# Optimization experiments

Hardware: AMD Instinct MI355X
Metric: run time of the kernel (lower is better)

The kernel has to match this reference:

```python
import jax, jax.numpy as jnp
import numpy as np

POOL = 7          # cfg.POOLING_SIZE
STRIDE = 16.0     # cfg.RPN_ANCHOR_STRIDE (y and x)


def _bilinear_sample(fm, py, px):
    """grid_sample (bilinear, zero padding, align_corners=True) for one image.
    fm: [C,H,W]; py, px: [R,Ho,Wo] pixel-space coords. Returns [C,R,Ho,Wo]."""
    C, H, W = fm.shape
    x0 = jnp.floor(px); y0 = jnp.floor(py)
    x1 = x0 + 1.0;      y1 = y0 + 1.0
    wx1 = px - x0; wx0 = 1.0 - wx1
    wy1 = py - y0; wy0 = 1.0 - wy1
    fm_flat = fm.reshape(C, H * W)

    def gather(y, x):
        valid = (x >= 0) & (x <= W - 1) & (y >= 0) & (y <= H - 1)
        xi = jnp.clip(x, 0, W - 1).astype(jnp.int32)
        yi = jnp.clip(y, 0, H - 1).astype(jnp.int32)
        v = jnp.take(fm_flat, (yi * W + xi).reshape(-1), axis=1)
        return v.reshape((C,) + y.shape) * valid.astype(fm.dtype)

    return (gather(y0, x0) * (wy0 * wx0) + gather(y0, x1) * (wy0 * wx1)
          + gather(y1, x0) * (wy1 * wx0) + gather(y1, x1) * (wy1 * wx1))


def setup_inputs() -> dict:
    key = jax.random.key(0)
    k1, k2, k3 = jax.random.split(key, 3)
    N, R, C, H, W = 4, 256, 1024, 50, 50
    # boxes (y, x, h, w) in original image coords (800x800 image, stride 16)
    yx = jax.random.uniform(k1, (N, R, 2), jnp.float32, 0.0, 600.0)
    hw = jax.random.uniform(k2, (N, R, 2), jnp.float32, 32.0, 200.0)
    rois = jnp.concatenate([yx, hw], axis=-1)
    feature_map = jax.random.normal(k3, (N, C, H, W), jnp.float32)
    return {"rois": rois, "feature_map": feature_map}


def reference(rois, feature_map):
    N, C, H, W = feature_map.shape
    R = rois.shape[1]
    y1 = rois[:, :, 0] / STRIDE
    x1 = rois[:, :, 1] / STRIDE
    y2 = (rois[:, :, 0] + rois[:, :, 2]) / STRIDE
    x2 = (rois[:, :, 1] + rois[:, :, 3]) / STRIDE
    # affine theta (align_corners=True convention, matching the (W-1) formulas)
    a  = (x2 - x1) / (W - 1)
    tx = (x1 + x2 - W + 1) / (W - 1)
    b  = (y2 - y1) / (H - 1)
    ty = (y1 + y2 - H + 1) / (H - 1)
    Ho = Wo = POOL * 2
    gx = jnp.linspace(-1.0, 1.0, Wo).astype(rois.dtype)
    gy = jnp.linspace(-1.0, 1.0, Ho).astype(rois.dtype)
    xs = a[:, :, None, None] * gx[None, None, None, :] + tx[:, :, None, None]  # [N,R,1,Wo]
    ys = b[:, :, None, None] * gy[None, None, :, None] + ty[:, :, None, None]  # [N,R,Ho,1]
    # normalized -> pixel coords (align_corners=True)
    px = jnp.broadcast_to((xs + 1.0) * (W - 1) / 2.0, (N, R, Ho, Wo))
    py = jnp.broadcast_to((ys + 1.0) * (H - 1) / 2.0, (N, R, Ho, Wo))
    sampled = jax.vmap(_bilinear_sample)(feature_map, py, px)  # [N,C,R,Ho,Wo]
    crops = jnp.transpose(sampled, (0, 2, 1, 3, 4))            # [N,R,C,Ho,Wo]
    crops = crops.reshape(N, R, C, POOL, 2, POOL, 2).max(axis=(4, 6))
    return crops  # [N,R,C,7,7]
```

## Files before the change

### kernel.cpp

```cpp
#include <hip/hip_runtime.h>
#include <math.h>

static constexpr int N_ = 4, R_ = 256, C_ = 1024, H_ = 50, W_ = 50, P_ = 7;
static constexpr int HW_ = H_ * W_;
static constexpr int PP_ = P_ * P_;
static constexpr int CHB_ = 4;
static constexpr int WVS_ = 16;
static constexpr int PLW_ = 2816;
static constexpr int NTASK = R_ * PP_;
static constexpr int NIT = NTASK / 64;
static constexpr int FM_WORDS = N_ * C_ * HW_;

typedef const __attribute__((address_space(1))) void* gaddr_t;
typedef __attribute__((address_space(3))) void* laddr_t;

__device__ __forceinline__ void ld_lds16(const float* g, float* l) {
    __builtin_amdgcn_global_load_lds((gaddr_t)g, (laddr_t)l, 16, 0, 0);
}

__device__ __forceinline__ void axis_w(float p0, float p1, int L,
                                       int& i0c, float wA[2], float wB[3]) {
    float f0 = floorf(p0); int i0 = (int)f0; float a0 = p0 - f0;
    float f1 = floorf(p1); int i1 = (int)f1; float a1 = p1 - f1;
    const bool o = (i1 > i0);
    wA[0] = 1.0f - a0; wA[1] = a0;
    wB[0] = o ? 0.0f : (1.0f - a1);
    wB[1] = o ? (1.0f - a1) : a1;
    wB[2] = o ? a1 : 0.0f;
    if (i0 > L - 1)     { wA[0] = 0.0f; wB[0] = 0.0f; }
    if (i0 + 1 > L - 1) { wA[1] = 0.0f; wB[1] = 0.0f; }
    if (i0 + 2 > L - 1) {               wB[2] = 0.0f; }
    i0c = min(max(i0, 0), L - 1);
}

__device__ __forceinline__ float gather9(const float* __restrict__ g,
                                         const float wyA[2], const float wyB[3],
                                         const float wxA[2], const float wxB[3]) {
    const float v00 = g[0],       v01 = g[1],          v02 = g[2];
    const float v10 = g[W_],      v11 = g[W_ + 1],     v12 = g[W_ + 2];
    const float v20 = g[2 * W_],  v21 = g[2 * W_ + 1], v22 = g[2 * W_ + 2];

    const float tA0 = fmaf(wyA[1], v10, wyA[0] * v00);
    const float tA1 = fmaf(wyA[1], v11, wyA[0] * v01);
    const float tA2 = fmaf(wyA[1], v12, wyA[0] * v02);
    const float tB0 = fmaf(wyB[2], v20, fmaf(wyB[1], v10, wyB[0] * v00));
    const float tB1 = fmaf(wyB[2], v21, fmaf(wyB[1], v11, wyB[0] * v01));
    const float tB2 = fmaf(wyB[2], v22, fmaf(wyB[1], v12, wyB[0] * v02));

    const float s00 = fmaf(wxA[1], tA1, wxA[0] * tA0);
    const float s01 = fmaf(wxB[2], tA2, fmaf(wxB[1], tA1, wxB[0] * tA0));
    const float s10 = fmaf(wxA[1], tB1, wxA[0] * tB0);
    const float s11 = fmaf(wxB[2], tB2, fmaf(wxB[1], tB1, wxB[0] * tB0));

    return fmaxf(fmaxf(s00, s01), fmaxf(s10, s11));
}

__global__ __launch_bounds__(1024, 8) void roipool_kernel(
    const float* __restrict__ rois,
    const float* __restrict__ fm,
    float* __restrict__ out) {

    __shared__ float planes[CHB_][PLW_];

    const int b  = blockIdx.x;
    const int n  = b >> 8;
    const int c0 = (b & 255) * CHB_;
    const int lane = threadIdx.x & 63;
    const int wv = __builtin_amdgcn_readfirstlane(threadIdx.x >> 6);

    {
        const int pl = wv >> 2;
        const int qh = wv & 3;
        const int base = (n * C_ + c0 + pl) * HW_;
        float* dst = &planes[pl][0];
        const int t0 = qh * 3, t1 = min(t0 + 3, 11);
        for (int t = t0; t < t1; ++t) {
            const int src = min(base + t * 256 + lane * 4, FM_WORDS - 4);
            ld_lds16(fm + src, dst + t * 256);
        }
    }
    asm volatile("s_waitcnt vmcnt(0)" ::: "memory");
    __syncthreads();

    const float* const p0l = &planes[0][0];
    const float* const p1l = &planes[1][0];
    const float* const p2l = &planes[2][0];
    const float* const p3l = &planes[3][0];

    const float4* __restrict__ rois4 = reinterpret_cast<const float4*>(rois) + n * R_;
    const size_t obase = ((size_t)n * R_ * C_ + c0) * PP_;

    for (int it = wv; it < NIT; it += WVS_) {
        const int t  = (it << 6) | lane;
        const int ri = (int)((unsigned)t / 49u);
        const int px = t - ri * 49;
        const int pi = (int)((unsigned)px / 7u);
        const int pj = px - pi * 7;

        const float4 roi = rois4[ri];
        const float y1 = roi.x * 0.0625f;
        const float x1 = roi.y * 0.0625f;
        const float y2 = (roi.x + roi.z) * 0.0625f;
        const float x2 = (roi.y + roi.w) * 0.0625f;
        const float sy = (y2 - y1) * (1.0f / 13.0f);
        const float sx = (x2 - x1) * (1.0f / 13.0f);

        const float py0 = y1 + sy * (float)(2 * pi);
        const float py1 = y1 + sy * (float)(2 * pi + 1);
        const float px0 = x1 + sx * (float)(2 * pj);
        const float px1 = x1 + sx * (float)(2 * pj + 1);

        int iy0; float wyA[2], wyB[3];
        axis_w(py0, py1, H_, iy0, wyA, wyB);
        int ix0; float wxA[2], wxB[3];
        axis_w(px0, px1, W_, ix0, wxA, wxB);
        const int gb = iy0 * W_ + ix0;

        const float r0 = gather9(p0l + gb, wyA, wyB, wxA, wxB);
        const float r1 = gather9(p1l + gb, wyA, wyB, wxA, wxB);
        const float r2 = gather9(p2l + gb, wyA, wyB, wxA, wxB);
        const float r3 = gather9(p3l + gb, wyA, wyB, wxA, wxB);

        float* __restrict__ po = out + obase + (size_t)ri * C_ * PP_ + px;
        po[0]       = r0;
        po[PP_]     = r1;
        po[2 * PP_] = r2;
        po[3 * PP_] = r3;
    }
}

extern "C" void kernel_launch(void* const* d_in, const int* in_sizes, int n_in,
                              void* d_out, int out_size, void* d_ws, size_t ws_size,
                              hipStream_t stream) {
    const float* rois = (const float*)d_in[0];
    const float* fm   = (const float*)d_in[1];
    float* out        = (float*)d_out;

    const int blocks = N_ * (C_ / CHB_);
    roipool_kernel<<<blocks, 1024, 0, stream>>>(rois, fm, out);
}
```

Measured before the change: 77.42 us.

## Interleave four channels as float4 in LDS and halve block size

Feature-map planes are staged in LDS interleaved by channel as float4, so each of the 9 taps is read with one 128-bit LDS load covering all four channels instead of four scalar loads. The async global_load_lds staging is replaced by ordinary strided global loads that the threads pack into float4 themselves. Block size drops from 1024 to 512 threads with 8 waves, which doubles the per-wave loop trip count. This trades a heavier, non-async staging phase for fewer LDS instructions in the gather loop.

```diff
diff --git a/kernel.cpp b/kernel.cpp
--- a/kernel.cpp
+++ b/kernel.cpp
@@ -5,18 +5,10 @@
 static constexpr int HW_ = H_ * W_;
 static constexpr int PP_ = P_ * P_;
 static constexpr int CHB_ = 4;
-static constexpr int WVS_ = 16;
-static constexpr int PLW_ = 2816;
+static constexpr int WVS_ = 8;
+static constexpr int P4_ = 2608;
 static constexpr int NTASK = R_ * PP_;
 static constexpr int NIT = NTASK / 64;
-static constexpr int FM_WORDS = N_ * C_ * HW_;
-
-typedef const __attribute__((address_space(1))) void* gaddr_t;
-typedef __attribute__((address_space(3))) void* laddr_t;
-
-__device__ __forceinline__ void ld_lds16(const float* g, float* l) {
-    __builtin_amdgcn_global_load_lds((gaddr_t)g, (laddr_t)l, 16, 0, 0);
-}
 
 __device__ __forceinline__ void axis_w(float p0, float p1, int L,
                                        int& i0c, float wA[2], float wB[3]) {
@@ -33,59 +25,33 @@
     i0c = min(max(i0, 0), L - 1);
 }
 
-__device__ __forceinline__ float gather9(const float* __restrict__ g,
-                                         const float wyA[2], const float wyB[3],
-                                         const float wxA[2], const float wxB[3]) {
-    const float v00 = g[0],       v01 = g[1],          v02 = g[2];
-    const float v10 = g[W_],      v11 = g[W_ + 1],     v12 = g[W_ + 2];
-    const float v20 = g[2 * W_],  v21 = g[2 * W_ + 1], v22 = g[2 * W_ + 2];
-
-    const float tA0 = fmaf(wyA[1], v10, wyA[0] * v00);
-    const float tA1 = fmaf(wyA[1], v11, wyA[0] * v01);
-    const float tA2 = fmaf(wyA[1], v12, wyA[0] * v02);
-    const float tB0 = fmaf(wyB[2], v20, fmaf(wyB[1], v10, wyB[0] * v00));
-    const float tB1 = fmaf(wyB[2], v21, fmaf(wyB[1], v11, wyB[0] * v01));
-    const float tB2 = fmaf(wyB[2], v22, fmaf(wyB[1], v12, wyB[0] * v02));
-
-    const float s00 = fmaf(wxA[1], tA1, wxA[0] * tA0);
-    const float s01 = fmaf(wxB[2], tA2, fmaf(wxB[1], tA1, wxB[0] * tA0));
-    const float s10 = fmaf(wxA[1], tB1, wxA[0] * tB0);
-    const float s11 = fmaf(wxB[2], tB2, fmaf(wxB[1], tB1, wxB[0] * tB0));
-
-    return fmaxf(fmaxf(s00, s01), fmaxf(s10, s11));
-}
-
-__global__ __launch_bounds__(1024, 8) void roipool_kernel(
+__global__ __launch_bounds__(512) void roipool_kernel(
     const float* __restrict__ rois,
     const float* __restrict__ fm,
     float* __restrict__ out) {
 
-    __shared__ float planes[CHB_][PLW_];
+    __shared__ float4 sh4[P4_];
 
     const int b  = blockIdx.x;
     const int n  = b >> 8;
     const int c0 = (b & 255) * CHB_;
-    const int lane = threadIdx.x & 63;
-    const int wv = __builtin_amdgcn_readfirstlane(threadIdx.x >> 6);
+    const int tid = threadIdx.x;
+    const int lane = tid & 63;
+    const int wv = __builtin_amdgcn_readfirstlane(tid >> 6);
 
     {
-        const int pl = wv >> 2;
-        const int qh = wv & 3;
-        const int base = (n * C_ + c0 + pl) * HW_;
-        float* dst = &planes[pl][0];
-        const int t0 = qh * 3, t1 = min(t0 + 3, 11);
-        for (int t = t0; t < t1; ++t) {
-            const int src = min(base + t * 256 + lane * 4, FM_WORDS - 4);
-            ld_lds16(fm + src, dst + t * 256);
+        const int gpb = (n * C_ + c0) * HW_;
+        for (int p = tid; p < P4_; p += 512) {
+            const int sp = min(p, HW_ - 1);
+            float4 v;
+            v.x = fm[gpb + sp];
+            v.y = fm[gpb + HW_ + sp];
+            v.z = fm[gpb + 2 * HW_ + sp];
+            v.w = fm[gpb + 3 * HW_ + sp];
+            sh4[p] = v;
         }
     }
-    asm volatile("s_waitcnt vmcnt(0)" ::: "memory");
     __syncthreads();
-
-    const float* const p0l = &planes[0][0];
-    const float* const p1l = &planes[1][0];
-    const float* const p2l = &planes[2][0];
-    const float* const p3l = &planes[3][0];
 
     const float4* __restrict__ rois4 = reinterpret_cast<const float4*>(rois) + n * R_;
     const size_t obase = ((size_t)n * R_ * C_ + c0) * PP_;
@@ -107,19 +73,39 @@
 
         const float py0 = y1 + sy * (float)(2 * pi);
         const float py1 = y1 + sy * (float)(2 * pi + 1);
-        const float px0 = x1 + sx * (float)(2 * pj);
-        const float px1 = x1 + sx * (float)(2 * pj + 1);
+        const float qx0 = x1 + sx * (float)(2 * pj);
+        const float qx1 = x1 + sx * (float)(2 * pj + 1);
 
         int iy0; float wyA[2], wyB[3];
         axis_w(py0, py1, H_, iy0, wyA, wyB);
         int ix0; float wxA[2], wxB[3];
-        axis_w(px0, px1, W_, ix0, wxA, wxB);
+        axis_w(qx0, qx1, W_, ix0, wxA, wxB);
         const int gb = iy0 * W_ + ix0;
 
-        const float r0 = gather9(p0l + gb, wyA, wyB, wxA, wxB);
-        const float r1 = gather9(p1l + gb, wyA, wyB, wxA, wxB);
-        const float r2 = gather9(p2l + gb, wyA, wyB, wxA, wxB);
-        const float r3 = gather9(p3l + gb, wyA, wyB, wxA, wxB);
+        const float4* __restrict__ G = sh4 + gb;
+        const float4 v00 = G[0],       v01 = G[1],          v02 = G[2];
+        const float4 v10 = G[W_],      v11 = G[W_ + 1],     v12 = G[W_ + 2];
+        const float4 v20 = G[2 * W_],  v21 = G[2 * W_ + 1], v22 = G[2 * W_ + 2];
+
+        float r0, r1, r2, r3;
+#define REDUCE_CH(CMP, RES) do {                                               \
+        const float tA0 = fmaf(wyA[1], v10.CMP, wyA[0] * v00.CMP);             \
+        const float tA1 = fmaf(wyA[1], v11.CMP, wyA[0] * v01.CMP);             \
+        const float tA2 = fmaf(wyA[1], v12.CMP, wyA[0] * v02.CMP);             \
+        const float tB0 = fmaf(wyB[2], v20.CMP, fmaf(wyB[1], v10.CMP, wyB[0] * v00.CMP)); \
+        const float tB1 = fmaf(wyB[2], v21.CMP, fmaf(wyB[1], v11.CMP, wyB[0] * v01.CMP)); \
+        const float tB2 = fmaf(wyB[2], v22.CMP, fmaf(wyB[1], v12.CMP, wyB[0] * v02.CMP)); \
+        const float s00 = fmaf(wxA[1], tA1, wxA[0] * tA0);                     \
+        const float s01 = fmaf(wxB[2], tA2, fmaf(wxB[1], tA1, wxB[0] * tA0));  \
+        const float s10 = fmaf(wxA[1], tB1, wxA[0] * tB0);                     \
+        const float s11 = fmaf(wxB[2], tB2, fmaf(wxB[1], tB1, wxB[0] * tB0));  \
+        RES = fmaxf(fmaxf(s00, s01), fmaxf(s10, s11));                         \
+    } while (0)
+        REDUCE_CH(x, r0);
+        REDUCE_CH(y, r1);
+        REDUCE_CH(z, r2);
+        REDUCE_CH(w, r3);
+#undef REDUCE_CH
 
         float* __restrict__ po = out + obase + (size_t)ri * C_ * PP_ + px;
         po[0]       = r0;
@@ -137,5 +123,5 @@
     float* out        = (float*)d_out;
 
     const int blocks = N_ * (C_ / CHB_);
-    roipool_kernel<<<blocks, 1024, 0, stream>>>(rois, fm, out);
+    roipool_kernel<<<blocks, 512, 0, stream>>>(rois, fm, out);
 }
```

Result: faster. 72.70 us (-6.1%).
